# Optimization experiments

Measured on AMD Instinct MI355X. Metric: run time of the kernel, lower is better.

## Reference

```python
import jax, jax.numpy as jnp
import numpy as np

NQ = 4          # qubits
NL = 4          # StronglyEntanglingLayers layers (weights.shape[0])
RANGES = [1, 2, 3, 1]  # PennyLane default ranges: (l % (NQ-1)) + 1
B = 1_000_000


def _apply_1q(psi, U, wire):
    # psi: [B,2,2,2,2] complex; U: [2,2] (shared) or [B,2,2] (per-sample)
    psi = jnp.moveaxis(psi, wire + 1, -1)
    if U.ndim == 3:
        psi = jnp.einsum('bji,b...i->b...j', U, psi)
    else:
        psi = jnp.einsum('ji,b...i->b...j', U, psi)
    return jnp.moveaxis(psi, -1, wire + 1)


def _cnot(psi, c, t):
    # flip target axis on the control=1 slice
    psi = jnp.moveaxis(psi, (c + 1, t + 1), (-2, -1))
    psi = jnp.stack([psi[..., 0, :], psi[..., 1, ::-1]], axis=-2)
    return jnp.moveaxis(psi, (-2, -1), (c + 1, t + 1))


def _rot(phi, theta, omega):
    # PennyLane Rot(phi,theta,omega) = RZ(omega) @ RY(theta) @ RZ(phi)
    c = jnp.cos(theta / 2).astype(jnp.complex64)
    s = jnp.sin(theta / 2).astype(jnp.complex64)
    epo = jnp.exp(-0.5j * (phi + omega).astype(jnp.complex64))
    emo = jnp.exp(0.5j * (phi - omega).astype(jnp.complex64))
    a = epo * c
    b = -emo * s
    d = jnp.conj(emo) * s
    e = jnp.conj(epo) * c
    return jnp.stack([jnp.stack([a, b]), jnp.stack([d, e])])  # [2,2]


def _circuit(x, weights):
    # batched 4-qubit state-vector sim; x: [B,4] angles, weights: [4,4,3]
    b = x.shape[0]
    psi = jnp.zeros((b, 2 ** NQ), jnp.complex64).at[:, 0].set(1.0)
    psi = psi.reshape((b,) + (2,) * NQ)
    # RX angle embedding (per-sample gates)
    half = x / 2
    c = jnp.cos(half).astype(jnp.complex64)
    s = (-1j) * jnp.sin(half).astype(jnp.complex64)
    for w in range(NQ):
        U = jnp.stack([jnp.stack([c[:, w], s[:, w]], -1),
                       jnp.stack([s[:, w], c[:, w]], -1)], -2)  # [B,2,2]
        psi = _apply_1q(psi, U, w)
    # StronglyEntanglingLayers: Rot on each wire, then ring of CNOTs
    for l in range(NL):
        for w in range(NQ):
            psi = _apply_1q(psi, _rot(weights[l, w, 0], weights[l, w, 1], weights[l, w, 2]), w)
        r = RANGES[l]
        for w in range(NQ):
            psi = _cnot(psi, w, (w + r) % NQ)
    # PauliZ expvals per wire
    probs = psi.real ** 2 + psi.imag ** 2  # [B,2,2,2,2]
    z = []
    for w in range(NQ):
        axes = tuple(a for a in range(1, NQ + 1) if a != w + 1)
        m = probs.sum(axes)  # [B,2]
        z.append(m[:, 0] - m[:, 1])
    return jnp.stack(z, -1).astype(jnp.float32)  # [B,4]


def setup_inputs() -> dict:
    key = jax.random.key(0)
    k1, k2, k3, k4 = jax.random.split(key, 4)
    x = jax.random.uniform(k1, (B, NQ), jnp.float32)
    weights = jax.random.uniform(k2, (NL, NQ, 3), jnp.float32)  # np.random.rand(4,4,3)
    fc_w = jax.random.normal(k3, (10, NQ), jnp.float32) * 0.5
    fc_b = jax.random.normal(k4, (10,), jnp.float32) * 0.1
    return {"x": x, "weights": weights, "fc_w": fc_w, "fc_b": fc_b}


def reference(x, weights, fc_w, fc_b):
    q = _circuit(x, weights)          # [B,4]
    return q @ fc_w.T + fc_b          # [B,10]
```

## Files before the change

### kernel.cpp

```cpp
#include <hip/hip_runtime.h>

#define NQ 4
#define NL 4

typedef _Float16 f16x8 __attribute__((ext_vector_type(8)));
typedef float f32x16 __attribute__((ext_vector_type(16)));

#define INV2PI 0.15915494309189535f
#define CHUNKS 4
#define CSAMP  256

__global__ __launch_bounds__(256) void qnn_fused(
    const float4* __restrict__ x,
    const float*  __restrict__ w,
    const float*  __restrict__ fcw,
    const float*  __restrict__ fcb,
    float*        __restrict__ out,
    int nB)
{
  __shared__ float  sM[512];
  __shared__ float  sG[512];
  __shared__ float4 xbuf[2][CSAMP];
  __shared__ float  obuf[2][CSAMP * 10];

  int t    = threadIdx.x;
  int lane = t & 63;
  int wv   = t >> 6;
  int col  = lane & 31;
  int hi   = lane >> 5;

  {
    int k = t >> 4;
    int j = t & 15;
    int gbase = lane & 48;

    float re = (j == k) ? 1.f : 0.f;
    float im = 0.f;

    const int ranges[4] = {1, 2, 3, 1};
#pragma unroll
    for (int l = 0; l < NL; ++l) {
#pragma unroll
      for (int q = 0; q < NQ; ++q) {
        float phi = w[l*12 + q*3 + 0];
        float th  = w[l*12 + q*3 + 1];
        float om  = w[l*12 + q*3 + 2];
        float st, ct;  __sincosf(0.5f*th, &st, &ct);
        float spo, cpo; __sincosf(0.5f*(phi+om), &spo, &cpo);
        float smo, cmo; __sincosf(0.5f*(phi-om), &smo, &cmo);
        float ar = cpo*ct,  ai = -spo*ct;
        float br = -cmo*st, bi = -smo*st;
        float dr = cmo*st,  di = -smo*st;
        float er = cpo*ct,  ei = spo*ct;

        int m = 8 >> q;
        float pre = __shfl_xor(re, m);
        float pim = __shfl_xor(im, m);
        bool one = (j & m) != 0;
        float scr = one ? er : ar, sci = one ? ei : ai;
        float pcr = one ? dr : br, pci = one ? di : bi;
        float nre = scr*re - sci*im + pcr*pre - pci*pim;
        float nim = scr*im + sci*re + pcr*pim + pci*pre;
        re = nre; im = nim;
      }
      int r = ranges[l];
      int src = j;
#pragma unroll
      for (int q = 3; q >= 0; --q) {
        int mc = 8 >> q;
        int mt = 8 >> ((q + r) & 3);
        src ^= (src & mc) ? mt : 0;
      }
      re = __shfl(re, gbase + src);
      im = __shfl(im, gbase + src);
    }

    int pc = __popc(k) & 3;
    float re2, im2;
    if      (pc == 0) { re2 =  re; im2 =  im; }
    else if (pc == 1) { re2 =  im; im2 = -re; }
    else if (pc == 2) { re2 = -re; im2 = -im; }
    else              { re2 = -im; im2 =  re; }
    sM[j*16 + k]        = re2;
    sM[(16 + j)*16 + k] = im2;

    if (t < 160) {
      int o  = t >> 4;
      int kk = t & 15;
      int jj = (kk & 3) + 8 * ((kk >> 2) & 1) + 4 * (kk >> 3);
      float g = fcw[o*4 + 0] * ((jj & 8) ? -1.f : 1.f)
              + fcw[o*4 + 1] * ((jj & 4) ? -1.f : 1.f)
              + fcw[o*4 + 2] * ((jj & 2) ? -1.f : 1.f)
              + fcw[o*4 + 3] * ((jj & 1) ? -1.f : 1.f);
      sG[t] = g;
    }
    for (int i = t; i < 352; i += 256) sG[160 + i] = 0.f;
  }
  __syncthreads();

  int row = col;
  int k0  = hi * 8;
  f16x8 Ahi, Alo, Ghi;
#pragma unroll
  for (int i = 0; i < 8; ++i) {
    float v = sM[row * 16 + k0 + i];
    _Float16 h = (_Float16)v;
    Ahi[i] = h;
    Alo[i] = (_Float16)(v - (float)h);
    Ghi[i] = (_Float16)sG[row * 16 + k0 + i];
  }

  int o0 = hi * 4;
  float b0 = fcb[o0 + 0], b1 = fcb[o0 + 1], b2 = fcb[o0 + 2], b3 = fcb[o0 + 3];
  float b4 = hi ? 0.f : fcb[8];
  float b5 = hi ? 0.f : fcb[9];

  int base = blockIdx.x * (CHUNKS * CSAMP);
  int lim  = nB * 10;

  {
    int s = base + t;
    float4 pv = x[(s < nB) ? s : (nB - 1)];
    xbuf[0][t] = pv;
  }
  __syncthreads();

#pragma unroll
  for (int c = 0; c < CHUNKS; ++c) {
    float4 nv;
    if (c + 1 < CHUNKS) {
      int s = base + (c + 1) * CSAMP + t;
      nv = x[(s < nB) ? s : (nB - 1)];
    }

    float* ob = obuf[c & 1];

#pragma unroll
    for (int g = 0; g < 2; ++g) {
      int sl = wv * 64 + g * 32 + col;
      float4 xv = xbuf[c & 1][sl];

      float rev0 = xv.x * (0.5f * INV2PI);
      float cs0  = __builtin_amdgcn_sinf(hi ? rev0 : rev0 + 0.25f);
      float rev1 = xv.y * (0.5f * INV2PI);
      float s1 = __builtin_amdgcn_sinf(rev1), c1 = __builtin_amdgcn_cosf(rev1);
      float rev2 = xv.z * (0.5f * INV2PI);
      float s2 = __builtin_amdgcn_sinf(rev2), c2 = __builtin_amdgcn_cosf(rev2);
      float rev3 = xv.w * (0.5f * INV2PI);
      float s3 = __builtin_amdgcn_sinf(rev3), c3 = __builtin_amdgcn_cosf(rev3);

      float a0 = cs0 * c1, a1 = cs0 * s1;
      float w0 = c2 * c3, w1 = c2 * s3, w2 = s2 * c3, w3 = s2 * s3;
      f16x8 Bf;
      Bf[0] = (_Float16)(a0 * w0); Bf[1] = (_Float16)(a0 * w1);
      Bf[2] = (_Float16)(a0 * w2); Bf[3] = (_Float16)(a0 * w3);
      Bf[4] = (_Float16)(a1 * w0); Bf[5] = (_Float16)(a1 * w1);
      Bf[6] = (_Float16)(a1 * w2); Bf[7] = (_Float16)(a1 * w3);

      f32x16 acc = {0.f,0.f,0.f,0.f,0.f,0.f,0.f,0.f,
                    0.f,0.f,0.f,0.f,0.f,0.f,0.f,0.f};
      acc = __builtin_amdgcn_mfma_f32_32x32x16_f16(Ahi, Bf, acc, 0, 0, 0);
      acc = __builtin_amdgcn_mfma_f32_32x32x16_f16(Alo, Bf, acc, 0, 0, 0);

      f16x8 Bp;
      Bp[0] = (_Float16)fmaf(acc[0], acc[0], acc[8]  * acc[8]);
      Bp[1] = (_Float16)fmaf(acc[1], acc[1], acc[9]  * acc[9]);
      Bp[2] = (_Float16)fmaf(acc[2], acc[2], acc[10] * acc[10]);
      Bp[3] = (_Float16)fmaf(acc[3], acc[3], acc[11] * acc[11]);
      Bp[4] = (_Float16)fmaf(acc[4], acc[4], acc[12] * acc[12]);
      Bp[5] = (_Float16)fmaf(acc[5], acc[5], acc[13] * acc[13]);
      Bp[6] = (_Float16)fmaf(acc[6], acc[6], acc[14] * acc[14]);
      Bp[7] = (_Float16)fmaf(acc[7], acc[7], acc[15] * acc[15]);

      f32x16 acc2 = {b0, b1, b2, b3, b4, b5, 0.f, 0.f,
                     0.f, 0.f, 0.f, 0.f, 0.f, 0.f, 0.f, 0.f};
      acc2 = __builtin_amdgcn_mfma_f32_32x32x16_f16(Ghi, Bp, acc2, 0, 0, 0);

      float2 v01; v01.x = acc2[0]; v01.y = acc2[1];
      float2 v23; v23.x = acc2[2]; v23.y = acc2[3];
      *(float2*)&ob[sl * 10 + o0]     = v01;
      *(float2*)&ob[sl * 10 + o0 + 2] = v23;
      if (!hi) {
        float2 v89; v89.x = acc2[4]; v89.y = acc2[5];
        *(float2*)&ob[sl * 10 + 8] = v89;
      }
    }

    if (c + 1 < CHUNKS) {
      xbuf[(c + 1) & 1][t] = nv;
    }
    __syncthreads();

    int cb = base * 10 + c * (CSAMP * 10);
#pragma unroll
    for (int i = 0; i < 3; ++i) {
      int idx = t + i * 256;
      if (idx < 640) {
        int gidx = cb + idx * 4;
        if (gidx < lim) {
          float4 v = *(float4*)&ob[idx * 4];
          *(float4*)&out[gidx] = v;
        }
      }
    }
  }
}

extern "C" void kernel_launch(void* const* d_in, const int* in_sizes, int n_in,
                              void* d_out, int out_size, void* d_ws, size_t ws_size,
                              hipStream_t stream) {
  const float* x   = (const float*)d_in[0];
  const float* w   = (const float*)d_in[1];
  const float* fcw = (const float*)d_in[2];
  const float* fcb = (const float*)d_in[3];
  float* out = (float*)d_out;
  int nB = in_sizes[0] / 4;

  int nblk = (nB + CHUNKS * CSAMP - 1) / (CHUNKS * CSAMP);
  hipLaunchKernelGGL(qnn_fused, dim3(nblk), dim3(256), 0, stream,
                     (const float4*)x, w, fcw, fcb, out, nB);
}
```

Before: 21.22 us.

## Write outputs directly to global, hoist x loads, halve chunks per block

Drops the LDS output staging buffer and its per-chunk barrier, so each lane stores its float2 results straight to global memory. Both chunks of x are loaded at kernel entry so their latency overlaps the unitary-matrix setup, and CHUNKS drops from 4 to 2, doubling the block count and shrinking LDS into one shared 8 KB array. The direct stores are strided, 8-byte and less coalesced than the earlier float4 staging path, which may cost bandwidth in exchange for fewer barriers and LDS traffic.

```diff
diff --git a/kernel.cpp b/kernel.cpp
--- a/kernel.cpp
+++ b/kernel.cpp
@@ -7,8 +7,8 @@
 typedef float f32x16 __attribute__((ext_vector_type(16)));
 
 #define INV2PI 0.15915494309189535f
-#define CHUNKS 4
 #define CSAMP  256
+#define CHUNKS 2
 
 __global__ __launch_bounds__(256) void qnn_fused(
     const float4* __restrict__ x,
@@ -18,16 +18,19 @@
     float*        __restrict__ out,
     int nB)
 {
-  __shared__ float  sM[512];
-  __shared__ float  sG[512];
-  __shared__ float4 xbuf[2][CSAMP];
-  __shared__ float  obuf[2][CSAMP * 10];
+  __shared__ float lds[2048];
 
   int t    = threadIdx.x;
   int lane = t & 63;
   int wv   = t >> 6;
   int col  = lane & 31;
   int hi   = lane >> 5;
+
+  int base = blockIdx.x * (CHUNKS * CSAMP);
+  int s0 = base + t;
+  int s1 = base + CSAMP + t;
+  float4 pv0 = x[(s0 < nB) ? s0 : (nB - 1)];
+  float4 pv1 = x[(s1 < nB) ? s1 : (nB - 1)];
 
   {
     int k = t >> 4;
@@ -81,8 +84,8 @@
     else if (pc == 1) { re2 =  im; im2 = -re; }
     else if (pc == 2) { re2 = -re; im2 = -im; }
     else              { re2 = -im; im2 =  re; }
-    sM[j*16 + k]        = re2;
-    sM[(16 + j)*16 + k] = im2;
+    lds[j*16 + k]        = re2;
+    lds[(16 + j)*16 + k] = im2;
 
     if (t < 160) {
       int o  = t >> 4;
@@ -92,9 +95,9 @@
               + fcw[o*4 + 1] * ((jj & 4) ? -1.f : 1.f)
               + fcw[o*4 + 2] * ((jj & 2) ? -1.f : 1.f)
               + fcw[o*4 + 3] * ((jj & 1) ? -1.f : 1.f);
-      sG[t] = g;
+      lds[512 + t] = g;
     }
-    for (int i = t; i < 352; i += 256) sG[160 + i] = 0.f;
+    for (int i = t; i < 352; i += 256) lds[512 + 160 + i] = 0.f;
   }
   __syncthreads();
 
@@ -103,11 +106,11 @@
   f16x8 Ahi, Alo, Ghi;
 #pragma unroll
   for (int i = 0; i < 8; ++i) {
-    float v = sM[row * 16 + k0 + i];
+    float v = lds[row * 16 + k0 + i];
     _Float16 h = (_Float16)v;
     Ahi[i] = h;
     Alo[i] = (_Float16)(v - (float)h);
-    Ghi[i] = (_Float16)sG[row * 16 + k0 + i];
+    Ghi[i] = (_Float16)lds[512 + row * 16 + k0 + i];
   }
 
   int o0 = hi * 4;
@@ -115,30 +118,20 @@
   float b4 = hi ? 0.f : fcb[8];
   float b5 = hi ? 0.f : fcb[9];
 
-  int base = blockIdx.x * (CHUNKS * CSAMP);
-  int lim  = nB * 10;
-
-  {
-    int s = base + t;
-    float4 pv = x[(s < nB) ? s : (nB - 1)];
-    xbuf[0][t] = pv;
-  }
   __syncthreads();
 
+  float4* xbuf = (float4*)lds;
+  xbuf[t]         = pv0;
+  xbuf[CSAMP + t] = pv1;
+  __syncthreads();
+
 #pragma unroll
   for (int c = 0; c < CHUNKS; ++c) {
-    float4 nv;
-    if (c + 1 < CHUNKS) {
-      int s = base + (c + 1) * CSAMP + t;
-      nv = x[(s < nB) ? s : (nB - 1)];
-    }
-
-    float* ob = obuf[c & 1];
-
 #pragma unroll
     for (int g = 0; g < 2; ++g) {
       int sl = wv * 64 + g * 32 + col;
-      float4 xv = xbuf[c & 1][sl];
+      int s  = base + c * CSAMP + sl;
+      float4 xv = xbuf[c * CSAMP + sl];
 
       float rev0 = xv.x * (0.5f * INV2PI);
       float cs0  = __builtin_amdgcn_sinf(hi ? rev0 : rev0 + 0.25f);
@@ -176,30 +169,15 @@
                      0.f, 0.f, 0.f, 0.f, 0.f, 0.f, 0.f, 0.f};
       acc2 = __builtin_amdgcn_mfma_f32_32x32x16_f16(Ghi, Bp, acc2, 0, 0, 0);
 
-      float2 v01; v01.x = acc2[0]; v01.y = acc2[1];
-      float2 v23; v23.x = acc2[2]; v23.y = acc2[3];
-      *(float2*)&ob[sl * 10 + o0]     = v01;
-      *(float2*)&ob[sl * 10 + o0 + 2] = v23;
-      if (!hi) {
-        float2 v89; v89.x = acc2[4]; v89.y = acc2[5];
-        *(float2*)&ob[sl * 10 + 8] = v89;
-      }
-    }
-
-    if (c + 1 < CHUNKS) {
-      xbuf[(c + 1) & 1][t] = nv;
-    }
-    __syncthreads();
-
-    int cb = base * 10 + c * (CSAMP * 10);
-#pragma unroll
-    for (int i = 0; i < 3; ++i) {
-      int idx = t + i * 256;
-      if (idx < 640) {
-        int gidx = cb + idx * 4;
-        if (gidx < lim) {
-          float4 v = *(float4*)&ob[idx * 4];
-          *(float4*)&out[gidx] = v;
+      if (s < nB) {
+        float* op = out + (size_t)s * 10 + o0;
+        float2 v01; v01.x = acc2[0]; v01.y = acc2[1];
+        float2 v23; v23.x = acc2[2]; v23.y = acc2[3];
+        *(float2*)(op + 0) = v01;
+        *(float2*)(op + 2) = v23;
+        if (!hi) {
+          float2 v89; v89.x = acc2[4]; v89.y = acc2[5];
+          *(float2*)(out + (size_t)s * 10 + 8) = v89;
         }
       }
     }
```

New measurement: 25.65 us. 1.21x slower.
